# Optimization experiments

Hardware: AMD Instinct MI355X
Metric: run time of the kernel (lower is better)

The kernel has to match this reference:

```python
import jax, jax.numpy as jnp
import numpy as np

K, S, P = 3, 2, 2  # kernel_size, stride, padding (dilation=1)


def _unfold(xp, k, s, oh, ow):
    """Extract k*k strided patches from a padded array.

    xp: (..., Hp, Wp) -> (..., k*k, oh, ow), window-position ordering (kh, kw)
    matching torch.nn.Unfold (channel-major handled by caller).
    """
    return jnp.stack(
        [xp[..., i:i + s * (oh - 1) + 1:s, j:j + s * (ow - 1) + 1:s]
         for i in range(K) for j in range(K)],
        axis=-3,
    )


def setup_inputs() -> dict:
    key = jax.random.key(0)
    x = jax.random.normal(key, (8, 256, 128, 128), dtype=jnp.float32)
    return {"x": x}


def reference(x):
    b, c, h, w = x.shape
    oh = (h - K + 2 * P) // S + 1
    ow = (w - K + 2 * P) // S + 1

    # channel-wise L2 norm, computed BEFORE unfolding (padding contributes 0 either way)
    n = jnp.sqrt(jnp.sum(x * x, axis=1))            # (b, h, w)
    n_pad = jnp.pad(n, ((0, 0), (P, P), (P, P)))
    n_patch = _unfold(n_pad, K, S, oh, ow)          # (b, k*k, oh, ow)
    # weighting_fn = softmax over the k*k window positions (torch dim=1 of unfolded norm)
    wts = jax.nn.softmax(n_patch, axis=1)           # (b, k*k, oh, ow)

    x_pad = jnp.pad(x, ((0, 0), (0, 0), (P, P), (P, P)))
    x_patch = _unfold(x_pad, K, S, oh, ow)          # (b, c, k*k, oh, ow)

    # weighted sum over window positions
    return jnp.sum(wts[:, None] * x_patch, axis=2)  # (b, c, oh, ow)
```

## Files before the change

kernel.cpp:

```cpp
#include <hip/hip_runtime.h>
#include <math.h>

#define BATCH 8
#define CH    256
#define H     128
#define W     128
#define HW    (H * W)
#define OH    65
#define OW    65
#define NPIX  (OH * OW)

__global__ __launch_bounds__(256) void norm_kernel(const float4* __restrict__ x4,
                                                   float* __restrict__ nrm) {
    const int b    = blockIdx.x >> 6;
    const int t    = blockIdx.x & 63;
    const int lane = threadIdx.x & 63;
    const int wv   = threadIdx.x >> 6;

    const float4* p = x4 + (size_t)(b * CH + wv * 64) * (HW / 4) + t * 64 + lane;
    float4 a = {0.f, 0.f, 0.f, 0.f};
    #pragma unroll 8
    for (int c = 0; c < 64; ++c) {
        float4 v = p[(size_t)c * (HW / 4)];
        a.x += v.x * v.x; a.y += v.y * v.y;
        a.z += v.z * v.z; a.w += v.w * v.w;
    }
    __shared__ float part[4][256];
    ((float4*)part[wv])[lane] = a;
    __syncthreads();
    float s = part[0][threadIdx.x] + part[1][threadIdx.x]
            + part[2][threadIdx.x] + part[3][threadIdx.x];
    nrm[(size_t)b * HW + t * 256 + threadIdx.x] = sqrtf(s);
}

#define K2TPB 256
#define CPW   32
#define CGC   128

__global__ __launch_bounds__(K2TPB) void pool_kernel(const float* __restrict__ x,
                                                     const float* __restrict__ nrm,
                                                     float* __restrict__ out) {
    const int b   = blockIdx.x & 7;
    const int rem = blockIdx.x >> 3;
    const int oh  = rem % OH;
    const int cg  = rem / OH;
    const int tid  = threadIdx.x;
    const int lane = tid & 63;
    const int wv   = tid >> 6;

    int  rowc[3];
    #pragma unroll
    for (int r = 0; r < 3; ++r) {
        int ih = oh * 2 + r - 2;
        rowc[r] = ih < 0 ? 0 : (ih > H - 1 ? H - 1 : ih);
    }

    __shared__ float ns[3][W];
    __shared__ float wls[OH][9];

    for (int id = tid; id < 3 * W; id += K2TPB) {
        int r = id >> 7, col = id & (W - 1);
        ns[r][col] = nrm[(size_t)b * HW + rowc[r] * W + col];
    }
    __syncthreads();

    if (tid < OH) {
        const int ow  = tid;
        const int iw0 = ow * 2 - 2;
        float nv[9]; bool val[9]; float m = 0.0f;
        #pragma unroll
        for (int kh = 0; kh < 3; ++kh) {
            int ih = oh * 2 + kh - 2;
            bool vh = (unsigned)ih < (unsigned)H;
            #pragma unroll
            for (int kw = 0; kw < 3; ++kw) {
                int iw = iw0 + kw;
                int k  = kh * 3 + kw;
                bool v = vh && ((unsigned)iw < (unsigned)W);
                val[k] = v;
                nv[k]  = v ? ns[kh][iw] : 0.0f;
                m = fmaxf(m, nv[k]);
            }
        }
        float denom = 0.0f, wt[9];
        #pragma unroll
        for (int k = 0; k < 9; ++k) {
            float e = __expf(nv[k] - m);
            denom += e;
            wt[k] = val[k] ? e : 0.0f;
        }
        float inv = 1.0f / denom;
        #pragma unroll
        for (int k = 0; k < 9; ++k) wls[ow][k] = wt[k] * inv;
    }
    __syncthreads();

    const float wA0 = wls[lane][2], wA1 = wls[lane][5], wA2 = wls[lane][8];
    const float wB0 = wls[lane + 1][0], wC0 = wls[lane + 1][1];
    const float wB1 = wls[lane + 1][3], wC1 = wls[lane + 1][4];
    const float wB2 = wls[lane + 1][6], wC2 = wls[lane + 1][7];

    const float2* xw2 = (const float2*)x
        + (size_t)(b * CH + cg * CGC + wv * CPW) * (HW / 2);
    const int base0 = rowc[0] * (W / 2) + lane;
    const int base1 = rowc[1] * (W / 2) + lane;
    const int base2 = rowc[2] * (W / 2) + lane;

    float* ob = out + (size_t)(b * CH + cg * CGC + wv * CPW) * NPIX
                    + (size_t)oh * OW;
    #pragma unroll 8
    for (int c = 0; c < CPW; ++c) {
        const size_t cb = (size_t)c * (HW / 2);
        float2 v0 = xw2[cb + base0];
        float2 v1 = xw2[cb + base1];
        float2 v2 = xw2[cb + base2];
        float S = wB0 * v0.x + wC0 * v0.y
                + wB1 * v1.x + wC1 * v1.y
                + wB2 * v2.x + wC2 * v2.y;
        float T = wA0 * v0.x + wA1 * v1.x + wA2 * v2.x;
        float Sp = __shfl_up(S, 1);
        float res = (lane == 0) ? T : T + Sp;
        float* oc = ob + (size_t)c * NPIX;
        oc[lane] = res;
        if (lane == 63) oc[64] = S;
    }
}

extern "C" void kernel_launch(void* const* d_in, const int* in_sizes, int n_in,
                              void* d_out, int out_size, void* d_ws, size_t ws_size,
                              hipStream_t stream) {
    const float* x = (const float*)d_in[0];
    float* out  = (float*)d_out;
    float* nbuf = (float*)d_ws;

    norm_kernel<<<512, 256, 0, stream>>>((const float4*)x, nbuf);
    pool_kernel<<<BATCH * OH * 2, K2TPB, 0, stream>>>(x, nbuf, out);
}
```

Measured before the change: 218.6 us.

## Precompute softmax weights and stream rows per channel with register reuse

Adds a weights kernel that computes the per-window softmax weights once per batch and output row, storing them in a lane-major workspace buffer. A new pool kernel assigns one wave per channel and walks all output rows, carrying the shared input row between consecutive output rows in registers. This avoids recomputing the softmax for every channel group and cuts repeated reads of the overlapping input rows. In exchange it adds a kernel launch, a round trip of the weight buffer through memory, and only 512 blocks with a long serial loop, which may limit latency hiding. The previous kernel is kept as a fallback for when the workspace is too small.

```diff
diff --git a/kernel.cpp b/kernel.cpp
--- a/kernel.cpp
+++ b/kernel.cpp
@@ -33,13 +33,103 @@
     nrm[(size_t)b * HW + t * 256 + threadIdx.x] = sqrtf(s);
 }
 
+__global__ __launch_bounds__(128) void weights_kernel(const float* __restrict__ nrm,
+                                                      float* __restrict__ wbuf) {
+    const int b  = blockIdx.x & 7;
+    const int oh = blockIdx.x >> 3;
+    const int t  = threadIdx.x;
+
+    __shared__ float ws[OH][9];
+    if (t < OH) {
+        const int ow  = t;
+        const int iw0 = ow * 2 - 2;
+        const float* nb = nrm + (size_t)b * HW;
+        float nv[9]; bool val[9]; float m = 0.0f;
+        #pragma unroll
+        for (int kh = 0; kh < 3; ++kh) {
+            int ih = oh * 2 + kh - 2;
+            bool vh = (unsigned)ih < (unsigned)H;
+            #pragma unroll
+            for (int kw = 0; kw < 3; ++kw) {
+                int iw = iw0 + kw;
+                int k  = kh * 3 + kw;
+                bool v = vh && ((unsigned)iw < (unsigned)W);
+                val[k] = v;
+                nv[k]  = v ? nb[ih * W + iw] : 0.0f;
+                m = fmaxf(m, nv[k]);
+            }
+        }
+        float denom = 0.0f, wt[9];
+        #pragma unroll
+        for (int k = 0; k < 9; ++k) {
+            float e = __expf(nv[k] - m);
+            denom += e;
+            wt[k] = val[k] ? e : 0.0f;
+        }
+        float inv = 1.0f / denom;
+        #pragma unroll
+        for (int k = 0; k < 9; ++k) ws[ow][k] = wt[k] * inv;
+    }
+    __syncthreads();
+
+    if (t < 64) {
+        float k0 = ws[t][2],     k1 = ws[t][5],     k2 = ws[t][8];
+        float k3 = ws[t + 1][0], k4 = ws[t + 1][1];
+        float k5 = ws[t + 1][3], k6 = ws[t + 1][4];
+        float k7 = ws[t + 1][6], k8 = ws[t + 1][7];
+        float* wp = wbuf + (size_t)(b * OH + oh) * 9 * 64 + t;
+        wp[0]   = k0; wp[64]  = k1; wp[128] = k2;
+        wp[192] = k3; wp[256] = k4; wp[320] = k5;
+        wp[384] = k6; wp[448] = k7; wp[512] = k8;
+    }
+}
+
+__global__ __launch_bounds__(256) void pool_stream_kernel(
+        const float* __restrict__ x, const float* __restrict__ wbuf,
+        float* __restrict__ out) {
+    const int b    = blockIdx.x & 7;
+    const int g    = blockIdx.x >> 3;
+    const int lane = threadIdx.x & 63;
+    const int wv   = threadIdx.x >> 6;
+    const int c    = g * 4 + wv;
+
+    const float2* xr = (const float2*)(x + (size_t)(b * CH + c) * HW);
+    float*        op = out + (size_t)(b * CH + c) * NPIX;
+    const float*  wb = wbuf + (size_t)b * OH * 9 * 64 + lane;
+
+    float2 v2 = xr[lane];
+    float2 v0 = v2, v1 = v2;
+
+    #pragma unroll 4
+    for (int oh = 0; oh < OH; ++oh) {
+        const float* wk = wb + oh * (9 * 64);
+        float k0 = wk[0],   k1 = wk[64],  k2 = wk[128];
+        float k3 = wk[192], k4 = wk[256], k5 = wk[320];
+        float k6 = wk[384], k7 = wk[448], k8 = wk[512];
+        if (oh > 0) {
+            v0 = v2;
+            v1 = xr[(2 * oh - 1) * 64 + lane];
+            int r2 = (2 * oh < H) ? 2 * oh : H - 1;
+            v2 = xr[r2 * 64 + lane];
+        }
+        float T = k0 * v0.x + k1 * v1.x + k2 * v2.x;
+        float S = k3 * v0.x + k4 * v0.y
+                + k5 * v1.x + k6 * v1.y
+                + k7 * v2.x + k8 * v2.y;
+        float Sp = __shfl_up(S, 1);
+        float res = (lane == 0) ? T : T + Sp;
+        op[oh * OW + lane] = res;
+        if (lane == 63) op[oh * OW + 64] = S;
+    }
+}
+
 #define K2TPB 256
 #define CPW   32
 #define CGC   128
 
-__global__ __launch_bounds__(K2TPB) void pool_kernel(const float* __restrict__ x,
-                                                     const float* __restrict__ nrm,
-                                                     float* __restrict__ out) {
+__global__ __launch_bounds__(K2TPB) void pool_inline_kernel(
+        const float* __restrict__ x, const float* __restrict__ nrm,
+        float* __restrict__ out) {
     const int b   = blockIdx.x & 7;
     const int rem = blockIdx.x >> 3;
     const int oh  = rem % OH;
@@ -133,6 +223,16 @@
     float* out  = (float*)d_out;
     float* nbuf = (float*)d_ws;
 
+    const size_t norm_bytes = (size_t)BATCH * HW * sizeof(float);
+    const size_t wbuf_bytes = (size_t)BATCH * OH * 9 * 64 * sizeof(float);
+
     norm_kernel<<<512, 256, 0, stream>>>((const float4*)x, nbuf);
-    pool_kernel<<<BATCH * OH * 2, K2TPB, 0, stream>>>(x, nbuf, out);
-}
+
+    if (ws_size >= norm_bytes + wbuf_bytes) {
+        float* wbuf = nbuf + (size_t)BATCH * HW;
+        weights_kernel<<<BATCH * OH, 128, 0, stream>>>(nbuf, wbuf);
+        pool_stream_kernel<<<512, 256, 0, stream>>>(x, wbuf, out);
+    } else {
+        pool_inline_kernel<<<BATCH * OH * 2, K2TPB, 0, stream>>>(x, nbuf, out);
+    }
+}
```

After: 231.6 us. 5.9% more time.

## Restructure pool kernel to sweep rows per channel with register row reuse

Applied to the files above, without the earlier changes.

Each wavefront now owns one channel and walks down all output rows, carrying the shared input row between consecutive output rows in registers instead of reloading three rows per block. Softmax weights are recomputed per wave from the norm rows loaded alongside, and neighbour columns come from lane shuffles, which removes the shared-memory weight table and block barriers. The cost is redundant softmax work in every channel wave (4x more exp per channel than before) and lower parallelism, with 512 blocks each running a serial 65-step loop whose latency may be poorly hidden.

```diff
diff --git a/kernel.cpp b/kernel.cpp
--- a/kernel.cpp
+++ b/kernel.cpp
@@ -33,96 +33,86 @@
     nrm[(size_t)b * HW + t * 256 + threadIdx.x] = sqrtf(s);
 }
 
-#define K2TPB 256
-#define CPW   32
-#define CGC   128
+__global__ __launch_bounds__(256) void pool_kernel(const float* __restrict__ x,
+                                                   const float* __restrict__ nrm,
+                                                   float* __restrict__ out) {
+    const int b    = blockIdx.x & 7;
+    const int g    = blockIdx.x >> 3;
+    const int lane = threadIdx.x & 63;
+    const int wv   = threadIdx.x >> 6;
+    const int c    = g * 4 + wv;
 
-__global__ __launch_bounds__(K2TPB) void pool_kernel(const float* __restrict__ x,
-                                                     const float* __restrict__ nrm,
-                                                     float* __restrict__ out) {
-    const int b   = blockIdx.x & 7;
-    const int rem = blockIdx.x >> 3;
-    const int oh  = rem % OH;
-    const int cg  = rem / OH;
-    const int tid  = threadIdx.x;
-    const int lane = tid & 63;
-    const int wv   = tid >> 6;
+    const float2* xr = (const float2*)(x + (size_t)(b * CH + c) * HW);
+    const float2* nr = (const float2*)(nrm + (size_t)b * HW);
+    float*        op = out + (size_t)(b * CH + c) * NPIX;
 
-    int  rowc[3];
-    #pragma unroll
-    for (int r = 0; r < 3; ++r) {
-        int ih = oh * 2 + r - 2;
-        rowc[r] = ih < 0 ? 0 : (ih > H - 1 ? H - 1 : ih);
-    }
+    float2 xv2 = xr[lane], nv2 = nr[lane];
+    float2 xv0 = xv2, xv1 = xv2;
+    float2 nv0 = nv2, nv1 = nv2;
 
-    __shared__ float ns[3][W];
-    __shared__ float wls[OH][9];
+    #pragma unroll 4
+    for (int oh = 0; oh < OH; ++oh) {
+        if (oh > 0) {
+            xv0 = xv2; nv0 = nv2;
+            const int r1 = 2 * oh - 1;
+            const int r2 = (2 * oh < H) ? 2 * oh : H - 1;
+            xv1 = xr[r1 * 64 + lane]; nv1 = nr[r1 * 64 + lane];
+            xv2 = xr[r2 * 64 + lane]; nv2 = nr[r2 * 64 + lane];
+        }
+        const bool rv0 = (oh > 0);
+        const bool rv2 = (oh < OH - 1);
+        const bool cOK = (lane < 63);
 
-    for (int id = tid; id < 3 * W; id += K2TPB) {
-        int r = id >> 7, col = id & (W - 1);
-        ns[r][col] = nrm[(size_t)b * HW + rowc[r] * W + col];
-    }
-    __syncthreads();
+        float nd0 = __shfl_down(nv0.x, 1);
+        float nd1 = __shfl_down(nv1.x, 1);
+        float nd2 = __shfl_down(nv2.x, 1);
 
-    if (tid < OH) {
-        const int ow  = tid;
-        const int iw0 = ow * 2 - 2;
-        float nv[9]; bool val[9]; float m = 0.0f;
-        #pragma unroll
-        for (int kh = 0; kh < 3; ++kh) {
-            int ih = oh * 2 + kh - 2;
-            bool vh = (unsigned)ih < (unsigned)H;
-            #pragma unroll
-            for (int kw = 0; kw < 3; ++kw) {
-                int iw = iw0 + kw;
-                int k  = kh * 3 + kw;
-                bool v = vh && ((unsigned)iw < (unsigned)W);
-                val[k] = v;
-                nv[k]  = v ? ns[kh][iw] : 0.0f;
-                m = fmaxf(m, nv[k]);
-            }
+        float n00 = rv0 ? nv0.x : 0.f, n01 = rv0 ? nv0.y : 0.f;
+        float n02 = (rv0 && cOK) ? nd0 : 0.f;
+        float n10 = rv0 ? nv1.x : 0.f, n11 = rv0 ? nv1.y : 0.f;
+        float n12 = (rv0 && cOK) ? nd1 : 0.f;
+        float n20 = rv2 ? nv2.x : 0.f, n21 = rv2 ? nv2.y : 0.f;
+        float n22 = (rv2 && cOK) ? nd2 : 0.f;
+
+        float m = 0.f;
+        m = fmaxf(m, n00); m = fmaxf(m, n01); m = fmaxf(m, n02);
+        m = fmaxf(m, n10); m = fmaxf(m, n11); m = fmaxf(m, n12);
+        m = fmaxf(m, n20); m = fmaxf(m, n21); m = fmaxf(m, n22);
+
+        float e00 = __expf(n00 - m), e01 = __expf(n01 - m), e02 = __expf(n02 - m);
+        float e10 = __expf(n10 - m), e11 = __expf(n11 - m), e12 = __expf(n12 - m);
+        float e20 = __expf(n20 - m), e21 = __expf(n21 - m), e22 = __expf(n22 - m);
+        float denom = e00 + e01 + e02 + e10 + e11 + e12 + e20 + e21 + e22;
+        float inv = 1.0f / denom;
+
+        float w00 = rv0 ? e00 * inv : 0.f, w01 = rv0 ? e01 * inv : 0.f;
+        float w02 = (rv0 && cOK) ? e02 * inv : 0.f;
+        float w10 = rv0 ? e10 * inv : 0.f, w11 = rv0 ? e11 * inv : 0.f;
+        float w12 = (rv0 && cOK) ? e12 * inv : 0.f;
+        float w20 = rv2 ? e20 * inv : 0.f, w21 = rv2 ? e21 * inv : 0.f;
+        float w22 = (rv2 && cOK) ? e22 * inv : 0.f;
+
+        float xd0 = __shfl_down(xv0.x, 1);
+        float xd1 = __shfl_down(xv1.x, 1);
+        float xd2 = __shfl_down(xv2.x, 1);
+
+        float o = w00 * xv0.x + w01 * xv0.y + w02 * xd0
+                + w10 * xv1.x + w11 * xv1.y + w12 * xd1
+                + w20 * xv2.x + w21 * xv2.y + w22 * xd2;
+        op[oh * OW + 1 + lane] = o;
+
+        if (lane == 0) {
+            float m0 = fmaxf(fmaxf(0.f, n00), fmaxf(n10, n20));
+            float q0 = __expf(n00 - m0);
+            float q1 = __expf(n10 - m0);
+            float q2 = __expf(n20 - m0);
+            float d0 = 6.f * __expf(0.f - m0) + q0 + q1 + q2;
+            float i0 = 1.0f / d0;
+            float t0 = rv0 ? q0 * i0 : 0.f;
+            float t1 = rv0 ? q1 * i0 : 0.f;
+            float t2 = rv2 ? q2 * i0 : 0.f;
+            op[oh * OW] = t0 * xv0.x + t1 * xv1.x + t2 * xv2.x;
         }
-        float denom = 0.0f, wt[9];
-        #pragma unroll
-        for (int k = 0; k < 9; ++k) {
-            float e = __expf(nv[k] - m);
-            denom += e;
-            wt[k] = val[k] ? e : 0.0f;
-        }
-        float inv = 1.0f / denom;
-        #pragma unroll
-        for (int k = 0; k < 9; ++k) wls[ow][k] = wt[k] * inv;
-    }
-    __syncthreads();
-
-    const float wA0 = wls[lane][2], wA1 = wls[lane][5], wA2 = wls[lane][8];
-    const float wB0 = wls[lane + 1][0], wC0 = wls[lane + 1][1];
-    const float wB1 = wls[lane + 1][3], wC1 = wls[lane + 1][4];
-    const float wB2 = wls[lane + 1][6], wC2 = wls[lane + 1][7];
-
-    const float2* xw2 = (const float2*)x
-        + (size_t)(b * CH + cg * CGC + wv * CPW) * (HW / 2);
-    const int base0 = rowc[0] * (W / 2) + lane;
-    const int base1 = rowc[1] * (W / 2) + lane;
-    const int base2 = rowc[2] * (W / 2) + lane;
-
-    float* ob = out + (size_t)(b * CH + cg * CGC + wv * CPW) * NPIX
-                    + (size_t)oh * OW;
-    #pragma unroll 8
-    for (int c = 0; c < CPW; ++c) {
-        const size_t cb = (size_t)c * (HW / 2);
-        float2 v0 = xw2[cb + base0];
-        float2 v1 = xw2[cb + base1];
-        float2 v2 = xw2[cb + base2];
-        float S = wB0 * v0.x + wC0 * v0.y
-                + wB1 * v1.x + wC1 * v1.y
-                + wB2 * v2.x + wC2 * v2.y;
-        float T = wA0 * v0.x + wA1 * v1.x + wA2 * v2.x;
-        float Sp = __shfl_up(S, 1);
-        float res = (lane == 0) ? T : T + Sp;
-        float* oc = ob + (size_t)c * NPIX;
-        oc[lane] = res;
-        if (lane == 63) oc[64] = S;
     }
 }
 
@@ -134,5 +124,5 @@
     float* nbuf = (float*)d_ws;
 
     norm_kernel<<<512, 256, 0, stream>>>((const float4*)x, nbuf);
-    pool_kernel<<<BATCH * OH * 2, K2TPB, 0, stream>>>(x, nbuf, out);
+    pool_kernel<<<512, 256, 0, stream>>>(x, nbuf, out);
 }
```

Result: slower. 236.3 us (+8.1%).
